# Performance work log

Measured on AMD Instinct MI355X. Metric: run time of the kernel, lower is better.

Reference implementation:

```python
import jax, jax.numpy as jnp
import numpy as np

NUM_ITERATIONS = 5
NUM_TERMS = 3  # (degree + 1) // 2 with degree = 5
INITIAL_SCALE = 1.1


def setup_inputs() -> dict:
    key = jax.random.key(0)
    k1, k2 = jax.random.split(key)
    X = jax.random.normal(k1, (64, 1024, 1024), dtype=jnp.float32)
    coefficients = jnp.array([3.4445, -4.7750, 2.0315], dtype=jnp.float32)
    return {"X": X, "coefficients": coefficients}


def reference(X, coefficients):
    # Normalize each matrix to Frobenius norm INITIAL_SCALE
    fro = jnp.sqrt(jnp.sum(X * X, axis=(-2, -1), keepdims=True))
    X = X / fro * INITIAL_SCALE
    for _ in range(NUM_ITERATIONS):
        # XTX = X^T X, shape [B, M, M]
        XTX = jnp.einsum('bji,bjk->bik', X, X)
        term = X
        acc = coefficients[0] * X
        for i in range(1, NUM_TERMS):
            term = jnp.einsum('bij,bjk->bik', term, XTX)  # X (X^T X)^i
            acc = acc + coefficients[i] * term
        X = acc
    return X
```

## Files before the change

### kernel.cpp

```cpp
#include <hip/hip_runtime.h>
#include <hip/hip_bf16.h>
#include <stdint.h>

typedef float f32x4 __attribute__((ext_vector_type(4)));
typedef short bf16x8 __attribute__((ext_vector_type(8)));

#define LDW 1024
#define BATCH_SH 20

__device__ __forceinline__ float b2f(__hip_bfloat16 h) { return __bfloat162float(h); }
__device__ __forceinline__ __hip_bfloat16 f2b(float f) { return __float2bfloat16(f); }

__global__ void k_partial(const float* __restrict__ xin, float* __restrict__ partials) {
  const int b = blockIdx.y, ch = blockIdx.x, t = threadIdx.x;
  const size_t base = ((size_t)b << BATCH_SH) + (size_t)ch * 16384;
  float s = 0.f;
#pragma unroll
  for (int i = 0; i < 16; ++i) {
    f32x4 v = *reinterpret_cast<const f32x4*>(xin + base + (size_t)(i * 256 + t) * 4);
    s += v[0] * v[0] + v[1] * v[1] + v[2] * v[2] + v[3] * v[3];
  }
#pragma unroll
  for (int off = 32; off; off >>= 1) s += __shfl_down(s, off);
  __shared__ float red[4];
  if ((t & 63) == 0) red[t >> 6] = s;
  __syncthreads();
  if (t == 0) partials[b * 64 + ch] = red[0] + red[1] + red[2] + red[3];
}

__global__ void k_scale(const float* __restrict__ partials, float* __restrict__ scales) {
  const int b = blockIdx.x, t = threadIdx.x;
  float s = partials[b * 64 + t];
#pragma unroll
  for (int off = 32; off; off >>= 1) s += __shfl_down(s, off);
  if (t == 0) scales[b] = 1.1f / sqrtf(s);
}

__global__ void k_scalesplit(const float* __restrict__ xin, const float* __restrict__ scales,
                             __hip_bfloat16* __restrict__ Xh, __hip_bfloat16* __restrict__ Xl,
                             __hip_bfloat16* __restrict__ XTh, __hip_bfloat16* __restrict__ XTl) {
  __shared__ float tile[64][65];
  const int b = blockIdx.z, tm = blockIdx.y, tn = blockIdx.x;
  const size_t boff = (size_t)b << BATCH_SH;
  const float s = scales[b];
  const int t = threadIdx.x, lr0 = t >> 6, lc = t & 63;
#pragma unroll
  for (int p = 0; p < 16; ++p) {
    const int lr = p * 4 + lr0;
    const size_t idx = boff + (size_t)(tm * 64 + lr) * LDW + tn * 64 + lc;
    const float v = xin[idx] * s;
    __hip_bfloat16 h = f2b(v);
    Xh[idx] = h;
    Xl[idx] = f2b(v - b2f(h));
    tile[lr][lc] = v;
  }
  __syncthreads();
#pragma unroll
  for (int p = 0; p < 16; ++p) {
    const int lr = p * 4 + lr0;
    const float v = tile[lc][lr];
    const size_t idx = boff + (size_t)(tn * 64 + lr) * LDW + tm * 64 + lc;
    __hip_bfloat16 h = f2b(v);
    XTh[idx] = h;
    XTl[idx] = f2b(v - b2f(h));
  }
}


#define LOADSTG(S)                                                                        \
  {                                                                                       \
    const int seg_ = (S) >> 4, k0_ = ((S) & 15) << 6;                                     \
    const __hip_bfloat16* pa_ = seg_ == 0 ? pa0 : seg_ == 1 ? pa1 : pa2;                  \
    const __hip_bfloat16* pb_ = seg_ == 0 ? pb0 : seg_ == 1 ? pb1 : pb2;                  \
    _Pragma("unroll") for (int it_ = 0; it_ < 4; ++it_) {                                 \
      const int r_ = it_ * 64 + srow;                                                     \
      sa[it_] = *reinterpret_cast<const bf16x8*>(pa_ + boff + (size_t)(rowA + r_) * LDW + \
                                                 k0_ + chnk * 8);                         \
      sb[it_] = *reinterpret_cast<const bf16x8*>(pb_ + boff + (size_t)(rowB + r_) * LDW + \
                                                 k0_ + chnk * 8);                         \
    }                                                                                     \
  }

#define DSWRITE(DB)                                                                       \
  {                                                                                       \
    char* wb_ = smem + (DB) * 65536;                                                      \
    _Pragma("unroll") for (int it_ = 0; it_ < 4; ++it_) {                                 \
      const int r_ = it_ * 64 + srow;                                                     \
      const int sl_ = (chnk ^ (r_ & 7)) << 4;                                             \
      *reinterpret_cast<bf16x8*>(wb_ + r_ * 128 + sl_) = sa[it_];                         \
      *reinterpret_cast<bf16x8*>(wb_ + 32768 + r_ * 128 + sl_) = sb[it_];                 \
    }                                                                                     \
  }

#define MFMA_PHASE(KK, BASE)                                                              \
  {                                                                                       \
    bf16x8 av[8], bv[4];                                                                  \
    _Pragma("unroll") for (int mi_ = 0; mi_ < 8; ++mi_)                                   \
        av[mi_] = *reinterpret_cast<const bf16x8*>(smem + (BASE) + offA[KK][mi_]);        \
    _Pragma("unroll") for (int ni_ = 0; ni_ < 4; ++ni_)                                   \
        bv[ni_] = *reinterpret_cast<const bf16x8*>(smem + (BASE) + offB[KK][ni_]);        \
    __builtin_amdgcn_s_setprio(1);                                                        \
    _Pragma("unroll") for (int mi_ = 0; mi_ < 8; ++mi_)                                   \
        _Pragma("unroll") for (int ni_ = 0; ni_ < 4; ++ni_)                               \
            acc[mi_][ni_] = __builtin_amdgcn_mfma_f32_16x16x32_bf16(                      \
                av[mi_], bv[ni_], acc[mi_][ni_], 0, 0, 0);                                \
    __builtin_amdgcn_s_setprio(0);                                                        \
  }

template <int MODE>
__global__ __launch_bounds__(512, 2) void k_gemm(
    const __hip_bfloat16* __restrict__ pa0, const __hip_bfloat16* __restrict__ pa1,
    const __hip_bfloat16* __restrict__ pa2, const __hip_bfloat16* __restrict__ pb0,
    const __hip_bfloat16* __restrict__ pb1, const __hip_bfloat16* __restrict__ pb2,
    __hip_bfloat16* oh, __hip_bfloat16* ol,
    __hip_bfloat16* oth, __hip_bfloat16* otl,
    float* __restrict__ of,
    const __hip_bfloat16* __restrict__ eh, const __hip_bfloat16* __restrict__ el,
    const float* __restrict__ coef) {
  __shared__ __align__(16) char smem[131072];
  const int t = threadIdx.x;
  const int w = t >> 6, l = t & 63;
  const int wr = w >> 2, wc = w & 3;
  const int srow = t >> 3, chnk = t & 7;

  const int nwg = gridDim.x, q = nwg >> 3, r8 = nwg & 7;
  const int xcd = blockIdx.x & 7, o = blockIdx.x >> 3;
  const int wgid = (xcd < r8 ? xcd * (q + 1) : r8 * (q + 1) + (xcd - r8) * q) + o;

  int bat, tm, tn;
  if constexpr (MODE == 3) {
    bat = wgid >> 4;
    const int tile = wgid & 15;
    tm = tile >> 2; tn = tile & 3;
  } else {
    bat = (int)((unsigned)wgid / 10u);
    const int tile = wgid - bat * 10;
    tm = (tile < 4) ? 0 : (tile < 7) ? 1 : (tile < 9) ? 2 : 3;
    tn = (tile < 4) ? tile : (tile < 7) ? (tile - 3) : (tile < 9) ? (tile - 5) : 3;
  }
  const size_t boff = (size_t)bat << BATCH_SH;
  const int rowA = tm * 256, rowB = tn * 256;

  f32x4 acc[8][4];
#pragma unroll
  for (int i = 0; i < 8; ++i)
#pragma unroll
    for (int j = 0; j < 4; ++j) acc[i][j] = (f32x4){0.f, 0.f, 0.f, 0.f};

  int offA[2][8], offB[2][4];
#pragma unroll
  for (int kk = 0; kk < 2; ++kk) {
    const int g = kk * 4 + (l >> 4);
#pragma unroll
    for (int mi = 0; mi < 8; ++mi) {
      const int rA = wr * 128 + mi * 16 + (l & 15);
      offA[kk][mi] = rA * 128 + ((g ^ (rA & 7)) << 4);
    }
#pragma unroll
    for (int ni = 0; ni < 4; ++ni) {
      const int rB = wc * 64 + ni * 16 + (l & 15);
      offB[kk][ni] = 32768 + rB * 128 + ((g ^ (rB & 7)) << 4);
    }
  }

  bf16x8 sa[4], sb[4];
  LOADSTG(0);
  DSWRITE(0);
  LOADSTG(1);
  asm volatile("s_waitcnt lgkmcnt(0)" ::: "memory");
  __builtin_amdgcn_sched_barrier(0);
  __builtin_amdgcn_s_barrier();
  __builtin_amdgcn_sched_barrier(0);

  for (int s = 0; s < 48; ++s) {
    const int base = (s & 1) * 65536;
    MFMA_PHASE(0, base);
    if (s + 1 < 48) DSWRITE((s & 1) ^ 1);
    if (s + 2 < 48) LOADSTG(s + 2);
    MFMA_PHASE(1, base);
    asm volatile("s_waitcnt lgkmcnt(0)" ::: "memory");
    __builtin_amdgcn_sched_barrier(0);
    __builtin_amdgcn_s_barrier();
    __builtin_amdgcn_sched_barrier(0);
  }

  float c0 = 0.f, c1 = 0.f, c2 = 0.f;
  if constexpr (MODE == 2) { c0 = coef[0]; c1 = coef[1]; c2 = coef[2]; }
  const int r0 = tm * 256 + wr * 128 + ((l >> 4) << 2);
  const int cb = tn * 256 + wc * 64 + (l & 15);
#pragma unroll
  for (int mi = 0; mi < 8; ++mi) {
#pragma unroll
    for (int ni = 0; ni < 4; ++ni) {
      const int ccol = cb + ni * 16;
#pragma unroll
      for (int j = 0; j < 4; ++j) {
        const int rrow = r0 + mi * 16 + j;
        const size_t idx = boff + (size_t)rrow * LDW + ccol;
        const size_t tix = boff + (size_t)ccol * LDW + rrow;
        float v = acc[mi][ni][j];
        if constexpr (MODE == 2)
          v = c2 * v + c1 * (b2f(eh[idx]) + b2f(el[idx])) + (rrow == ccol ? c0 : 0.f);
        __hip_bfloat16 h = f2b(v);
        __hip_bfloat16 lo = f2b(v - b2f(h));
        if constexpr (MODE == 3) {
          if (oh) {
            oh[idx] = h; ol[idx] = lo;
            oth[tix] = h; otl[tix] = lo;
          }
          if (of) of[idx] = v;
        } else {
          oh[idx] = h; ol[idx] = lo;
          if (tm != tn) { oth[tix] = h; otl[tix] = lo; }
        }
      }
    }
  }
}

extern "C" void kernel_launch(void* const* d_in, const int* in_sizes, int n_in,
                              void* d_out, int out_size, void* d_ws, size_t ws_size,
                              hipStream_t stream) {
  (void)in_sizes; (void)n_in; (void)out_size;
  const float* xin = (const float*)d_in[0];
  const float* coef = (const float*)d_in[1];
  float* xout = (float*)d_out;

  int CH = 64;
  while (CH > 1 && ((size_t)CH * 16u * 1024u * 1024u + 65536u) > ws_size) CH >>= 1;

  const size_t nE = (size_t)CH << BATCH_SH;
  __hip_bfloat16* P0h = (__hip_bfloat16*)d_ws;
  __hip_bfloat16* P0l = P0h + nE;
  __hip_bfloat16* P1h = P0l + nE;
  __hip_bfloat16* P1l = P1h + nE;
  __hip_bfloat16* P2h = P1l + nE;
  __hip_bfloat16* P2l = P2h + nE;
  __hip_bfloat16* XTh = P2l + nE;
  __hip_bfloat16* XTl = XTh + nE;
  float* partials = (float*)(XTl + nE);
  float* scales = partials + (size_t)CH * 64;

  for (int c = 0; c < 64; c += CH) {
    const float* xi = xin + ((size_t)c << BATCH_SH);
    float* X = xout + ((size_t)c << BATCH_SH);
    k_partial<<<dim3(64, CH), 256, 0, stream>>>(xi, partials);
    k_scale<<<dim3(CH), 64, 0, stream>>>(partials, scales);
    k_scalesplit<<<dim3(16, 16, CH), 256, 0, stream>>>(xi, scales, P0h, P0l, XTh, XTl);

    __hip_bfloat16 *Xh = P0h, *Xl = P0l, *Ah = P1h, *Al = P1l, *Bh = P2h, *Bl = P2l;
    for (int it = 0; it < 5; ++it) {
      k_gemm<1><<<dim3(CH * 10), 512, 0, stream>>>(XTh, XTh, XTl, XTh, XTl, XTh,
                                                   Ah, Al, Ah, Al, nullptr,
                                                   nullptr, nullptr, nullptr);
      k_gemm<2><<<dim3(CH * 10), 512, 0, stream>>>(Ah, Ah, Al, Ah, Al, Ah,
                                                   Bh, Bl, Bh, Bl, nullptr,
                                                   Ah, Al, coef);
      k_gemm<3><<<dim3(CH * 16), 512, 0, stream>>>(Xh, Xh, Xl, Bh, Bl, Bh,
                                                   (it < 4) ? Ah : nullptr,
                                                   (it < 4) ? Al : nullptr,
                                                   XTh, XTl,
                                                   (it == 4) ? X : nullptr,
                                                   nullptr, nullptr, nullptr);
      __hip_bfloat16 *th = Xh, *tl = Xl;
      Xh = Ah; Xl = Al;
      Ah = Bh; Al = Bl;
      Bh = th; Bl = tl;
    }
  }
}
```

Before: 7.784 ms.

## Split GEMM main loop into four barrier-fenced phases interleaving LDS and global traffic

The GEMM K-loop iteration is split into four sub-phases, each covering half the M fragments for one k-half. Each sub-phase reads its A fragments (and B fragments once per k-half), writes one slice of the next stage into LDS, issues one slice of the following stage's global loads, then runs 16 MFMAs between workgroup barriers. The aim is to spread LDS writes and global loads evenly across the MFMA work and to hold fewer A-fragment registers at once. In exchange it adds eight barriers per iteration instead of one, which can stall waves and reduce overlap.

```diff
diff --git a/kernel.cpp b/kernel.cpp
--- a/kernel.cpp
+++ b/kernel.cpp
@@ -67,44 +67,61 @@
 }
 
 
-#define LOADSTG(S)                                                                        \
+#define SEGPTRS(S)                                                                        \
+  const int seg_ = (S) >> 4, k0_ = ((S) & 15) << 6;                                       \
+  const __hip_bfloat16* pa_ = seg_ == 0 ? pa0 : seg_ == 1 ? pa1 : pa2;                    \
+  const __hip_bfloat16* pb_ = seg_ == 0 ? pb0 : seg_ == 1 ? pb1 : pb2;
+
+#define LOAD_SLICE(S, P)                                                                  \
   {                                                                                       \
-    const int seg_ = (S) >> 4, k0_ = ((S) & 15) << 6;                                     \
-    const __hip_bfloat16* pa_ = seg_ == 0 ? pa0 : seg_ == 1 ? pa1 : pa2;                  \
-    const __hip_bfloat16* pb_ = seg_ == 0 ? pb0 : seg_ == 1 ? pb1 : pb2;                  \
-    _Pragma("unroll") for (int it_ = 0; it_ < 4; ++it_) {                                 \
-      const int r_ = it_ * 64 + srow;                                                     \
-      sa[it_] = *reinterpret_cast<const bf16x8*>(pa_ + boff + (size_t)(rowA + r_) * LDW + \
-                                                 k0_ + chnk * 8);                         \
-      sb[it_] = *reinterpret_cast<const bf16x8*>(pb_ + boff + (size_t)(rowB + r_) * LDW + \
-                                                 k0_ + chnk * 8);                         \
-    }                                                                                     \
-  }
-
-#define DSWRITE(DB)                                                                       \
+    SEGPTRS(S)                                                                            \
+    const int r_ = (P) * 64 + srow;                                                       \
+    sa[P] = *reinterpret_cast<const bf16x8*>(pa_ + boff + (size_t)(rowA + r_) * LDW +     \
+                                             k0_ + chnk * 8);                             \
+    sb[P] = *reinterpret_cast<const bf16x8*>(pb_ + boff + (size_t)(rowB + r_) * LDW +     \
+                                             k0_ + chnk * 8);                             \
+  }
+
+#define DSW_SLICE(DB, P)                                                                  \
   {                                                                                       \
     char* wb_ = smem + (DB) * 65536;                                                      \
-    _Pragma("unroll") for (int it_ = 0; it_ < 4; ++it_) {                                 \
-      const int r_ = it_ * 64 + srow;                                                     \
-      const int sl_ = (chnk ^ (r_ & 7)) << 4;                                             \
-      *reinterpret_cast<bf16x8*>(wb_ + r_ * 128 + sl_) = sa[it_];                         \
-      *reinterpret_cast<bf16x8*>(wb_ + 32768 + r_ * 128 + sl_) = sb[it_];                 \
-    }                                                                                     \
-  }
-
-#define MFMA_PHASE(KK, BASE)                                                              \
+    const int r_ = (P) * 64 + srow;                                                       \
+    const int sl_ = (chnk ^ (r_ & 7)) << 4;                                               \
+    *reinterpret_cast<bf16x8*>(wb_ + r_ * 128 + sl_) = sa[P];                             \
+    *reinterpret_cast<bf16x8*>(wb_ + 32768 + r_ * 128 + sl_) = sb[P];                     \
+  }
+
+#define DSREAD_AV(KK, MH)                                                                 \
+  _Pragma("unroll") for (int i_ = 0; i_ < 4; ++i_)                                        \
+      av[i_] = *reinterpret_cast<const bf16x8*>(smem + base + offA[KK][(MH) * 4 + i_]);
+
+#define DSREAD_BV(KK)                                                                     \
+  _Pragma("unroll") for (int i_ = 0; i_ < 4; ++i_)                                        \
+      bv[i_] = *reinterpret_cast<const bf16x8*>(smem + base + offB[KK][i_]);
+
+#define MFMA16(MH)                                                                        \
+  __builtin_amdgcn_s_setprio(1);                                                          \
+  _Pragma("unroll") for (int mi_ = 0; mi_ < 4; ++mi_)                                     \
+      _Pragma("unroll") for (int ni_ = 0; ni_ < 4; ++ni_)                                 \
+          acc[(MH) * 4 + mi_][ni_] = __builtin_amdgcn_mfma_f32_16x16x32_bf16(             \
+              av[mi_], bv[ni_], acc[(MH) * 4 + mi_][ni_], 0, 0, 0);                       \
+  __builtin_amdgcn_s_setprio(0);
+
+#define BAR() __builtin_amdgcn_s_barrier()
+#define LGKM0()                                       \
+  asm volatile("s_waitcnt lgkmcnt(0)" ::: "memory"); \
+  __builtin_amdgcn_sched_barrier(0)
+
+#define PHASE(KK, MH, P)                                                                  \
   {                                                                                       \
-    bf16x8 av[8], bv[4];                                                                  \
-    _Pragma("unroll") for (int mi_ = 0; mi_ < 8; ++mi_)                                   \
-        av[mi_] = *reinterpret_cast<const bf16x8*>(smem + (BASE) + offA[KK][mi_]);        \
-    _Pragma("unroll") for (int ni_ = 0; ni_ < 4; ++ni_)                                   \
-        bv[ni_] = *reinterpret_cast<const bf16x8*>(smem + (BASE) + offB[KK][ni_]);        \
-    __builtin_amdgcn_s_setprio(1);                                                        \
-    _Pragma("unroll") for (int mi_ = 0; mi_ < 8; ++mi_)                                   \
-        _Pragma("unroll") for (int ni_ = 0; ni_ < 4; ++ni_)                               \
-            acc[mi_][ni_] = __builtin_amdgcn_mfma_f32_16x16x32_bf16(                      \
-                av[mi_], bv[ni_], acc[mi_][ni_], 0, 0, 0);                                \
-    __builtin_amdgcn_s_setprio(0);                                                        \
+    if ((MH) == 0) { DSREAD_BV(KK); }                                                     \
+    DSREAD_AV(KK, MH);                                                                    \
+    if (wr_ok) DSW_SLICE(wdb, P);                                                         \
+    if (ld_ok) LOAD_SLICE(s + 2, P);                                                      \
+    BAR();                                                                                \
+    LGKM0();                                                                              \
+    MFMA16(MH);                                                                           \
+    BAR();                                                                                \
   }
 
 template <int MODE>
@@ -164,24 +181,25 @@
   }
 
   bf16x8 sa[4], sb[4];
-  LOADSTG(0);
-  DSWRITE(0);
-  LOADSTG(1);
-  asm volatile("s_waitcnt lgkmcnt(0)" ::: "memory");
-  __builtin_amdgcn_sched_barrier(0);
-  __builtin_amdgcn_s_barrier();
-  __builtin_amdgcn_sched_barrier(0);
+#pragma unroll
+  for (int p = 0; p < 4; ++p) LOAD_SLICE(0, p);
+#pragma unroll
+  for (int p = 0; p < 4; ++p) DSW_SLICE(0, p);
+#pragma unroll
+  for (int p = 0; p < 4; ++p) LOAD_SLICE(1, p);
+  LGKM0();
+  BAR();
 
   for (int s = 0; s < 48; ++s) {
     const int base = (s & 1) * 65536;
-    MFMA_PHASE(0, base);
-    if (s + 1 < 48) DSWRITE((s & 1) ^ 1);
-    if (s + 2 < 48) LOADSTG(s + 2);
-    MFMA_PHASE(1, base);
-    asm volatile("s_waitcnt lgkmcnt(0)" ::: "memory");
-    __builtin_amdgcn_sched_barrier(0);
-    __builtin_amdgcn_s_barrier();
-    __builtin_amdgcn_sched_barrier(0);
+    const int wdb = (s & 1) ^ 1;
+    const bool wr_ok = (s + 1 < 48);
+    const bool ld_ok = (s + 2 < 48);
+    bf16x8 av[4], bv[4];
+    PHASE(0, 0, 0)
+    PHASE(0, 1, 1)
+    PHASE(1, 0, 2)
+    PHASE(1, 1, 3)
   }
 
   float c0 = 0.f, c1 = 0.f, c2 = 0.f;
```

Result: slower. 8.337 ms (+7.1%).

## Load GEMM tiles directly from global to LDS with global_load_lds

Applied to the files above, without the earlier changes.

Replaces the register-staged global load plus ds_write double-buffer scheme with direct global-to-LDS 16-byte loads (global_load_lds). The XOR swizzle moves from the LDS write address to the global column index. The goal is to cut VGPR pressure and LDS write instructions. In exchange, prefetch depth drops from two stages ahead to one, and each iteration now waits on vmcnt(0) before the barrier, which may expose global memory latency.

```diff
diff --git a/kernel.cpp b/kernel.cpp
--- a/kernel.cpp
+++ b/kernel.cpp
@@ -10,6 +10,12 @@
 
 __device__ __forceinline__ float b2f(__hip_bfloat16 h) { return __bfloat162float(h); }
 __device__ __forceinline__ __hip_bfloat16 f2b(float f) { return __float2bfloat16(f); }
+
+__device__ __forceinline__ void gload16(const void* g, void* l) {
+  __builtin_amdgcn_global_load_lds((const __attribute__((address_space(1))) void*)g,
+                                   (__attribute__((address_space(3))) void*)l,
+                                   16, 0, 0);
+}
 
 __global__ void k_partial(const float* __restrict__ xin, float* __restrict__ partials) {
   const int b = blockIdx.y, ch = blockIdx.x, t = threadIdx.x;
@@ -67,28 +73,22 @@
 }
 
 
-#define LOADSTG(S)                                                                        \
+#define SEGPTRS(S)                                                                        \
+  const int seg_ = (S) >> 4, k0_ = ((S) & 15) << 6;                                       \
+  const __hip_bfloat16* pa_ = seg_ == 0 ? pa0 : seg_ == 1 ? pa1 : pa2;                    \
+  const __hip_bfloat16* pb_ = seg_ == 0 ? pb0 : seg_ == 1 ? pb1 : pb2;
+
+#define STAGE_GL(DB, S)                                                                   \
   {                                                                                       \
-    const int seg_ = (S) >> 4, k0_ = ((S) & 15) << 6;                                     \
-    const __hip_bfloat16* pa_ = seg_ == 0 ? pa0 : seg_ == 1 ? pa1 : pa2;                  \
-    const __hip_bfloat16* pb_ = seg_ == 0 ? pb0 : seg_ == 1 ? pb1 : pb2;                  \
+    SEGPTRS(S)                                                                            \
+    char* lb_ = smem + (DB) * 65536;                                                      \
     _Pragma("unroll") for (int it_ = 0; it_ < 4; ++it_) {                                 \
-      const int r_ = it_ * 64 + srow;                                                     \
-      sa[it_] = *reinterpret_cast<const bf16x8*>(pa_ + boff + (size_t)(rowA + r_) * LDW + \
-                                                 k0_ + chnk * 8);                         \
-      sb[it_] = *reinterpret_cast<const bf16x8*>(pb_ + boff + (size_t)(rowB + r_) * LDW + \
-                                                 k0_ + chnk * 8);                         \
-    }                                                                                     \
-  }
-
-#define DSWRITE(DB)                                                                       \
-  {                                                                                       \
-    char* wb_ = smem + (DB) * 65536;                                                      \
-    _Pragma("unroll") for (int it_ = 0; it_ < 4; ++it_) {                                 \
-      const int r_ = it_ * 64 + srow;                                                     \
-      const int sl_ = (chnk ^ (r_ & 7)) << 4;                                             \
-      *reinterpret_cast<bf16x8*>(wb_ + r_ * 128 + sl_) = sa[it_];                         \
-      *reinterpret_cast<bf16x8*>(wb_ + 32768 + r_ * 128 + sl_) = sb[it_];                 \
+      const int r_ = it_ * 64 + w * 8 + (l >> 3);                                         \
+      const int kx_ = k0_ + (((l & 7) ^ (l >> 3)) << 3);                                  \
+      gload16(pa_ + boff + (size_t)(rowA + r_) * LDW + kx_,                               \
+              lb_ + (it_ * 64 + w * 8) * 128 + l * 16);                                   \
+      gload16(pb_ + boff + (size_t)(rowB + r_) * LDW + kx_,                               \
+              lb_ + 32768 + (it_ * 64 + w * 8) * 128 + l * 16);                           \
     }                                                                                     \
   }
 
@@ -121,7 +121,6 @@
   const int t = threadIdx.x;
   const int w = t >> 6, l = t & 63;
   const int wr = w >> 2, wc = w & 3;
-  const int srow = t >> 3, chnk = t & 7;
 
   const int nwg = gridDim.x, q = nwg >> 3, r8 = nwg & 7;
   const int xcd = blockIdx.x & 7, o = blockIdx.x >> 3;
@@ -163,22 +162,19 @@
     }
   }
 
-  bf16x8 sa[4], sb[4];
-  LOADSTG(0);
-  DSWRITE(0);
-  LOADSTG(1);
-  asm volatile("s_waitcnt lgkmcnt(0)" ::: "memory");
+  STAGE_GL(0, 0);
+  asm volatile("s_waitcnt vmcnt(0)" ::: "memory");
   __builtin_amdgcn_sched_barrier(0);
   __builtin_amdgcn_s_barrier();
   __builtin_amdgcn_sched_barrier(0);
 
   for (int s = 0; s < 48; ++s) {
     const int base = (s & 1) * 65536;
+    if (s + 1 < 48) STAGE_GL((s & 1) ^ 1, s + 1);
+    __builtin_amdgcn_sched_barrier(0);
     MFMA_PHASE(0, base);
-    if (s + 1 < 48) DSWRITE((s & 1) ^ 1);
-    if (s + 2 < 48) LOADSTG(s + 2);
     MFMA_PHASE(1, base);
-    asm volatile("s_waitcnt lgkmcnt(0)" ::: "memory");
+    asm volatile("s_waitcnt vmcnt(0) lgkmcnt(0)" ::: "memory");
     __builtin_amdgcn_sched_barrier(0);
     __builtin_amdgcn_s_barrier();
     __builtin_amdgcn_sched_barrier(0);
```

Measured after the change: 7.895 ms. Within noise of the previous version (+1.4%).
